# Kernel optimization log

Measured on AMD Instinct MI355X. Metric: run time of the kernel, lower is better.

Reference implementation:

```python
import jax, jax.numpy as jnp
import numpy as np

HID = 128
N_LAYERS = 4
IN_DIM = 2


def _gru_layer(x_seq, W_ih, W_hh, b_ih, b_hh):
    """PyTorch-equivalent single GRU layer.
    x_seq: (T, N, F); W_ih: (3H, F); W_hh: (3H, H); b_ih, b_hh: (3H,)
    Gate order (PyTorch): r, z, n.
    """
    T, N, _ = x_seq.shape
    # precompute input projections for all timesteps: (T, N, 3H)
    gi = jnp.einsum('tnf,gf->tng', x_seq, W_ih) + b_ih

    def step(h, gi_t):
        gh = h @ W_hh.T + b_hh                      # (N, 3H)
        gi_r, gi_z, gi_n = jnp.split(gi_t, 3, axis=-1)
        gh_r, gh_z, gh_n = jnp.split(gh, 3, axis=-1)
        r = jax.nn.sigmoid(gi_r + gh_r)
        z = jax.nn.sigmoid(gi_z + gh_z)
        n = jnp.tanh(gi_n + r * gh_n)
        h_new = (1.0 - z) * n + z * h
        return h_new, h_new

    h0 = jnp.zeros((N, HID), dtype=x_seq.dtype)
    _, out = jax.lax.scan(step, h0, gi)
    return out                                       # (T, N, H)


def setup_inputs() -> dict:
    key = jax.random.key(0)
    ks = jax.random.split(key, 12)
    s = 1.0 / np.sqrt(HID)  # PyTorch GRU init scale
    x = jax.random.normal(ks[0], (512, IN_DIM, 1024), dtype=jnp.float32)
    W_ih0 = jax.random.uniform(ks[1], (3 * HID, IN_DIM), minval=-s, maxval=s)
    W_ih_rest = jax.random.uniform(ks[2], (N_LAYERS - 1, 3 * HID, HID), minval=-s, maxval=s)
    W_hh = jax.random.uniform(ks[3], (N_LAYERS, 3 * HID, HID), minval=-s, maxval=s)
    b_ih = jax.random.uniform(ks[4], (N_LAYERS, 3 * HID), minval=-s, maxval=s)
    b_hh = jax.random.uniform(ks[5], (N_LAYERS, 3 * HID), minval=-s, maxval=s)
    fc1_w = jax.random.uniform(ks[6], (HID, HID), minval=-s, maxval=s)
    fc1_b = jax.random.uniform(ks[7], (HID,), minval=-s, maxval=s)
    fc2_w = jax.random.uniform(ks[8], (3, HID), minval=-s, maxval=s)
    fc2_b = jax.random.uniform(ks[9], (3,), minval=-s, maxval=s)
    return {"x": x, "W_ih0": W_ih0, "W_ih_rest": W_ih_rest, "W_hh": W_hh,
            "b_ih": b_ih, "b_hh": b_hh, "fc1_w": fc1_w, "fc1_b": fc1_b,
            "fc2_w": fc2_w, "fc2_b": fc2_b}


def reference(x, W_ih0, W_ih_rest, W_hh, b_ih, b_hh, fc1_w, fc1_b, fc2_w, fc2_b):
    # x: (B, 2, S) -> transpose(1,2) -> (B, S, 2); GRU (batch_first=False)
    # treats axis0 as time T=B, axis1 as batch N=S.
    h = jnp.transpose(x, (0, 2, 1))                  # (T, N, 2)
    h = _gru_layer(h, W_ih0, W_hh[0], b_ih[0], b_hh[0])
    for l in range(1, N_LAYERS):
        h = _gru_layer(h, W_ih_rest[l - 1], W_hh[l], b_ih[l], b_hh[l])
    # out[:, -1, :] -> last lane along the GRU batch axis: (T, H)
    last = h[:, -1, :]
    hidden = jax.nn.relu(last @ fc1_w.T + fc1_b)
    return hidden @ fc2_w.T + fc2_b                  # (B, 3)
```

## Files before the change

kernel.cpp:

```cpp
#include <hip/hip_runtime.h>
#include <math.h>

#define T_SEQ  512
#define HID    128
#define G3     384
#define NL     4
#define CHUNK  8
#define NCHUNK (T_SEQ / CHUNK)

#define GI_TOT   (NL * T_SEQ * G3)
#define SEQ_TOT  (NL * T_SEQ * HID)
#define FLAG_OFF (GI_TOT + SEQ_TOT)

__device__ __forceinline__ float fsig(float x) {
    float e = __expf(-x);
    return 1.0f / (1.0f + e);
}
__device__ __forceinline__ float ftanh(float x) {
    float ax = fabsf(x);
    float e = __expf(-2.0f * ax);
    float t = (1.0f - e) / (1.0f + e);
    return copysignf(t, x);
}
__device__ __forceinline__ float rdlane(float v, int k) {
    return __uint_as_float(__builtin_amdgcn_readlane(__float_as_uint(v), k));
}


__global__ void init_flags(int* fl) {
    int i = threadIdx.x;
    if (i < 8) fl[i * 16] = (i == 0) ? NCHUNK : 0;
}

__global__ void gi0_kernel(const float* __restrict__ x, const float* __restrict__ Wih0,
                           const float* __restrict__ bih, float* __restrict__ gi) {
    int t = blockIdx.x;
    int g = threadIdx.x;
    float x0 = x[t * 2048 + 1023];
    float x1 = x[t * 2048 + 1024 + 1023];
    gi[t * G3 + g] = bih[g] + Wih0[g * 2 + 0] * x0 + Wih0[g * 2 + 1] * x1;
}

__global__ __launch_bounds__(256, 1) void pipe_kernel(float* __restrict__ ws,
                                                      const float* __restrict__ WihR,
                                                      const float* __restrict__ bih,
                                                      const float* __restrict__ Whh,
                                                      const float* __restrict__ bhh) {
    __shared__ float smem[12288];

    int bid  = blockIdx.x;
    int tid  = threadIdx.x;
    int lane = tid & 63;
    int q    = tid >> 6;
    int row0 = lane * 6;
    int* fl = (int*)(ws + FLAG_OFF);
    bool is_rec = (bid & 1) == 0;
    int  l      = is_rec ? (bid >> 1) : ((bid + 1) >> 1);

    if (is_rec) {
        const float* W   = Whh + (size_t)l * G3 * HID;
        const float* gi  = ws + (size_t)l * T_SEQ * G3;
        float* seq_o     = ws + GI_TOT + (size_t)l * T_SEQ * HID;
        float* aux       = smem + 3072;
        int* in_flag     = &fl[l * 16];
        int* out_flag    = &fl[(4 + l) * 16];

        float w[6][32];
        const float* wbase = W + q * 32;
#pragma unroll
        for (int i = 0; i < 6; i++) {
            const float4* wr = reinterpret_cast<const float4*>(wbase + (size_t)(row0 + i) * HID);
#pragma unroll
            for (int c = 0; c < 8; c++) {
                float4 v = wr[c];
                w[i][c * 4 + 0] = v.x; w[i][c * 4 + 1] = v.y;
                w[i][c * 4 + 2] = v.z; w[i][c * 4 + 3] = v.w;
            }
        }

        int  m  = lane & 31;
        bool p2 = (lane < 32);
        int  j  = q * 32 + m;
        const float* bb = bhh + (size_t)l * G3;
        float br = 0.f, bz = 0.f, bn = 0.f;
        if (p2) { br = bb[j]; bz = bb[HID + j]; bn = bb[2 * HID + j]; }

        float hs[32];
#pragma unroll
        for (int k = 0; k < 32; k++) hs[k] = 0.f;
        float hprev = 0.f;
        float g_r[CHUNK], g_z[CHUNK], g_n[CHUNK];
        int   fseen = 0;

        if (tid == 0) {
            while (__hip_atomic_fetch_add(in_flag, 0, __ATOMIC_RELAXED, __HIP_MEMORY_SCOPE_AGENT) < 1)
                __builtin_amdgcn_s_sleep(2);
        }
        __syncthreads();
        if (p2) {
            const float* gp = gi + j;
#pragma unroll
            for (int s = 0; s < CHUNK; s++) {
                g_r[s] = gp[s * G3];
                g_z[s] = gp[s * G3 + HID];
                g_n[s] = gp[s * G3 + 2 * HID];
            }
        }

        for (int c = 0; c < NCHUNK; c++) {
            int t0 = c * CHUNK;
            bool more = (c + 1 < NCHUNK);
#pragma unroll
            for (int s = 0; s < CHUNK; s++) {
                int t = t0 + s;
                float* psb = smem + (t & 1) * 1536;
                float acc[6];
#pragma unroll
                for (int i = 0; i < 6; i++) {
                    float a0 = 0.f, a1 = 0.f, a2 = 0.f, a3 = 0.f;
#pragma unroll
                    for (int k = 0; k < 32; k += 4) {
                        a0 += w[i][k]     * hs[k];
                        a1 += w[i][k + 1] * hs[k + 1];
                        a2 += w[i][k + 2] * hs[k + 2];
                        a3 += w[i][k + 3] * hs[k + 3];
                    }
                    acc[i] = (a0 + a1) + (a2 + a3);
                }
#pragma unroll
                for (int i = 0; i < 6; i += 2) {
                    float2 p; p.x = acc[i]; p.y = acc[i + 1];
                    *reinterpret_cast<float2*>(&psb[q * G3 + row0 + i]) = p;
                }
                __syncthreads();
                float hn_bc = 0.f;
                if (p2) {
                    float ghr = (psb[j]         + psb[G3 + j])         + (psb[2*G3 + j]         + psb[3*G3 + j]);
                    float ghz = (psb[HID + j]   + psb[G3 + HID + j])   + (psb[2*G3 + HID + j]   + psb[3*G3 + HID + j]);
                    float ghn = (psb[2*HID + j] + psb[G3 + 2*HID + j]) + (psb[2*G3 + 2*HID + j] + psb[3*G3 + 2*HID + j]);
                    float r = fsig(g_r[s] + ghr + br);
                    float z = fsig(g_z[s] + ghz + bz);
                    float n = ftanh(g_n[s] + r * (ghn + bn));
                    float hn = (1.0f - z) * n + z * hprev;
                    hprev = hn;
                    aux[s * HID + j] = hn;
                    hn_bc = hn;
                }
#pragma unroll
                for (int k = 0; k < 32; k++) hs[k] = rdlane(hn_bc, k);
            }
            __syncthreads();
            if (more && tid == 0)
                fseen = __hip_atomic_fetch_add(in_flag, 0, __ATOMIC_RELAXED, __HIP_MEMORY_SCOPE_AGENT);
            {
                float4 v = *reinterpret_cast<const float4*>(&aux[tid * 4]);
                *reinterpret_cast<float4*>(&seq_o[(size_t)t0 * HID + tid * 4]) = v;
            }
            __syncthreads();
            if (tid == 0)
                __hip_atomic_store(out_flag, c + 1, __ATOMIC_RELEASE, __HIP_MEMORY_SCOPE_AGENT);
            if (more && tid == 0) {
                while (fseen < c + 2) {
                    __builtin_amdgcn_s_sleep(2);
                    fseen = __hip_atomic_fetch_add(in_flag, 0, __ATOMIC_RELAXED, __HIP_MEMORY_SCOPE_AGENT);
                }
            }
            __syncthreads();
            if (more && p2) {
                const float* gp = gi + (size_t)(t0 + CHUNK) * G3 + j;
#pragma unroll
                for (int s = 0; s < CHUNK; s++) {
                    g_r[s] = gp[s * G3];
                    g_z[s] = gp[s * G3 + HID];
                    g_n[s] = gp[s * G3 + 2 * HID];
                }
            }
        }
    } else {
        const float* W   = WihR + (size_t)(l - 1) * G3 * HID;
        const float* seq_in = ws + GI_TOT + (size_t)(l - 1) * T_SEQ * HID;
        float* gi_o      = ws + (size_t)l * T_SEQ * G3;
        int* in_flag     = &fl[(4 + (l - 1)) * 16];
        int* out_flag    = &fl[l * 16];

        float w[6][32];
        const float* wbase = W + q * 32;
#pragma unroll
        for (int i = 0; i < 6; i++) {
            const float4* wr = reinterpret_cast<const float4*>(wbase + (size_t)(row0 + i) * HID);
#pragma unroll
            for (int c = 0; c < 8; c++) {
                float4 v = wr[c];
                w[i][c * 4 + 0] = v.x; w[i][c * 4 + 1] = v.y;
                w[i][c * 4 + 2] = v.z; w[i][c * 4 + 3] = v.w;
            }
        }
        int m  = lane & 31;
        int m2 = tid & 31;
        int s2 = tid >> 5;
        const float* bb = bih + (size_t)l * G3;
        float br4[4], bz4[4], bn4[4];
#pragma unroll
        for (int u = 0; u < 4; u++) {
            int jj = u * 32 + m2;
            br4[u] = bb[jj]; bz4[u] = bb[HID + jj]; bn4[u] = bb[2 * HID + jj];
        }

        for (int c = 0; c < NCHUNK; c++) {
            if (tid == 0) {
                while (__hip_atomic_fetch_add(in_flag, 0, __ATOMIC_RELAXED, __HIP_MEMORY_SCOPE_AGENT) < c + 1)
                    __builtin_amdgcn_s_sleep(2);
            }
            __syncthreads();
            int t0 = c * CHUNK;
            float vseq[CHUNK];
            {
                const float* sp = seq_in + (size_t)t0 * HID + q * 32 + m;
#pragma unroll
                for (int s = 0; s < CHUNK; s++) vseq[s] = sp[s * HID];
            }
#pragma unroll
            for (int s = 0; s < CHUNK; s++) {
                float xs[32];
#pragma unroll
                for (int k = 0; k < 32; k++) xs[k] = rdlane(vseq[s], k);
                float acc[6];
#pragma unroll
                for (int i = 0; i < 6; i++) {
                    float a0 = 0.f, a1 = 0.f, a2 = 0.f, a3 = 0.f;
#pragma unroll
                    for (int k = 0; k < 32; k += 4) {
                        a0 += w[i][k]     * xs[k];
                        a1 += w[i][k + 1] * xs[k + 1];
                        a2 += w[i][k + 2] * xs[k + 2];
                        a3 += w[i][k + 3] * xs[k + 3];
                    }
                    acc[i] = (a0 + a1) + (a2 + a3);
                }
                float* pp = smem + s * 1536;
#pragma unroll
                for (int i = 0; i < 6; i += 2) {
                    float2 p; p.x = acc[i]; p.y = acc[i + 1];
                    *reinterpret_cast<float2*>(&pp[q * G3 + row0 + i]) = p;
                }
            }
            __syncthreads();
#pragma unroll
            for (int u = 0; u < 4; u++) {
                int jj = u * 32 + m2;
                const float* pp = smem + s2 * 1536;
                float vr = (pp[jj]         + pp[G3 + jj])         + (pp[2*G3 + jj]         + pp[3*G3 + jj]);
                float vz = (pp[HID + jj]   + pp[G3 + HID + jj])   + (pp[2*G3 + HID + jj]   + pp[3*G3 + HID + jj]);
                float vn = (pp[2*HID + jj] + pp[G3 + 2*HID + jj]) + (pp[2*G3 + 2*HID + jj] + pp[3*G3 + 2*HID + jj]);
                float* gp = gi_o + (size_t)(t0 + s2) * G3;
                gp[jj]           = vr + br4[u];
                gp[HID + jj]     = vz + bz4[u];
                gp[2 * HID + jj] = vn + bn4[u];
            }
            __syncthreads();
            if (tid == 0)
                __hip_atomic_store(out_flag, c + 1, __ATOMIC_RELEASE, __HIP_MEMORY_SCOPE_AGENT);
        }
    }
}

__global__ void fc_kernel(const float* __restrict__ seq, const float* __restrict__ fc1w,
                          const float* __restrict__ fc1b, const float* __restrict__ fc2w,
                          const float* __restrict__ fc2b, float* __restrict__ out) {
    __shared__ float h3[HID];
    __shared__ float hid[HID];
    int t = blockIdx.x;
    int i = threadIdx.x;
    h3[i] = seq[t * HID + i];
    __syncthreads();
    const float4* w4 = reinterpret_cast<const float4*>(fc1w + i * HID);
    const float4* h4 = reinterpret_cast<const float4*>(h3);
    float a0 = 0.f, a1 = 0.f, a2 = 0.f, a3 = 0.f;
#pragma unroll
    for (int k = 0; k < 32; k += 4) {
        float4 w0 = w4[k], w1 = w4[k + 1], w2 = w4[k + 2], w3 = w4[k + 3];
        float4 h0 = h4[k], h1 = h4[k + 1], h2 = h4[k + 2], h3v = h4[k + 3];
        a0 += w0.x * h0.x + w0.y * h0.y + w0.z * h0.z + w0.w * h0.w;
        a1 += w1.x * h1.x + w1.y * h1.y + w1.z * h1.z + w1.w * h1.w;
        a2 += w2.x * h2.x + w2.y * h2.y + w2.z * h2.z + w2.w * h2.w;
        a3 += w3.x * h3v.x + w3.y * h3v.y + w3.z * h3v.z + w3.w * h3v.w;
    }
    float v = fc1b[i] + ((a0 + a1) + (a2 + a3));
    hid[i] = v > 0.0f ? v : 0.0f;
    __syncthreads();
    if (i < 3) {
        const float* w = fc2w + i * HID;
        float s = 0.f;
#pragma unroll
        for (int k = 0; k < HID; k++) s += w[k] * hid[k];
        out[t * 3 + i] = fc2b[i] + s;
    }
}

extern "C" void kernel_launch(void* const* d_in, const int* in_sizes, int n_in,
                              void* d_out, int out_size, void* d_ws, size_t ws_size,
                              hipStream_t stream) {
    const float* x     = (const float*)d_in[0];
    const float* Wih0  = (const float*)d_in[1];
    const float* WihR  = (const float*)d_in[2];
    const float* Whh   = (const float*)d_in[3];
    const float* bih   = (const float*)d_in[4];
    const float* bhh   = (const float*)d_in[5];
    const float* fc1w  = (const float*)d_in[6];
    const float* fc1b  = (const float*)d_in[7];
    const float* fc2w  = (const float*)d_in[8];
    const float* fc2b  = (const float*)d_in[9];
    float* out = (float*)d_out;
    float* ws  = (float*)d_ws;

    int*   flags = (int*)(ws + FLAG_OFF);
    float* gi0   = ws;
    float* seq3  = ws + GI_TOT + (size_t)3 * T_SEQ * HID;

    init_flags<<<1, 64, 0, stream>>>(flags);
    gi0_kernel<<<T_SEQ, G3, 0, stream>>>(x, Wih0, bih, gi0);
    pipe_kernel<<<7, 256, 0, stream>>>(ws, WihR, bih, Whh, bhh);
    fc_kernel<<<T_SEQ, HID, 0, stream>>>(seq3, fc1w, fc1b, fc2w, fc2b, out);
}
```

Baseline: 390.0 us.

## Double pipeline block width to 512 threads, halving per-thread matvec rows

Each block in the layer-pipelined GRU kernel now runs 8 wavefronts instead of 4. The 384 gate rows are split into two halves of 192, so each thread holds 3 weight rows instead of 6, and the GEMV store, aux write and gi_o reduction mappings are adjusted to match. The goal is to shorten the serial per-timestep matvec latency on the recurrence critical path by spreading the work across more waves. In exchange, each __syncthreads now covers twice as many waves, and the gate-update step runs redundantly in both halves.

```diff
diff --git a/kernel.cpp b/kernel.cpp
--- a/kernel.cpp
+++ b/kernel.cpp
@@ -41,7 +41,7 @@
     gi[t * G3 + g] = bih[g] + Wih0[g * 2 + 0] * x0 + Wih0[g * 2 + 1] * x1;
 }
 
-__global__ __launch_bounds__(256, 1) void pipe_kernel(float* __restrict__ ws,
+__global__ __launch_bounds__(512, 1) void pipe_kernel(float* __restrict__ ws,
                                                       const float* __restrict__ WihR,
                                                       const float* __restrict__ bih,
                                                       const float* __restrict__ Whh,
@@ -51,8 +51,10 @@
     int bid  = blockIdx.x;
     int tid  = threadIdx.x;
     int lane = tid & 63;
-    int q    = tid >> 6;
-    int row0 = lane * 6;
+    int wv   = tid >> 6;
+    int q    = wv & 3;
+    int half = wv >> 2;
+    int row0 = half * 192 + lane * 3;
     int* fl = (int*)(ws + FLAG_OFF);
     bool is_rec = (bid & 1) == 0;
     int  l      = is_rec ? (bid >> 1) : ((bid + 1) >> 1);
@@ -65,10 +67,10 @@
         int* in_flag     = &fl[l * 16];
         int* out_flag    = &fl[(4 + l) * 16];
 
-        float w[6][32];
+        float w[3][32];
         const float* wbase = W + q * 32;
 #pragma unroll
-        for (int i = 0; i < 6; i++) {
+        for (int i = 0; i < 3; i++) {
             const float4* wr = reinterpret_cast<const float4*>(wbase + (size_t)(row0 + i) * HID);
 #pragma unroll
             for (int c = 0; c < 8; c++) {
@@ -114,9 +116,9 @@
             for (int s = 0; s < CHUNK; s++) {
                 int t = t0 + s;
                 float* psb = smem + (t & 1) * 1536;
-                float acc[6];
-#pragma unroll
-                for (int i = 0; i < 6; i++) {
+                float acc[3];
+#pragma unroll
+                for (int i = 0; i < 3; i++) {
                     float a0 = 0.f, a1 = 0.f, a2 = 0.f, a3 = 0.f;
 #pragma unroll
                     for (int k = 0; k < 32; k += 4) {
@@ -128,10 +130,7 @@
                     acc[i] = (a0 + a1) + (a2 + a3);
                 }
 #pragma unroll
-                for (int i = 0; i < 6; i += 2) {
-                    float2 p; p.x = acc[i]; p.y = acc[i + 1];
-                    *reinterpret_cast<float2*>(&psb[q * G3 + row0 + i]) = p;
-                }
+                for (int i = 0; i < 3; i++) psb[q * G3 + row0 + i] = acc[i];
                 __syncthreads();
                 float hn_bc = 0.f;
                 if (p2) {
@@ -143,7 +142,7 @@
                     float n = ftanh(g_n[s] + r * (ghn + bn));
                     float hn = (1.0f - z) * n + z * hprev;
                     hprev = hn;
-                    aux[s * HID + j] = hn;
+                    if (half == 0) aux[s * HID + j] = hn;
                     hn_bc = hn;
                 }
 #pragma unroll
@@ -153,8 +152,8 @@
             if (more && tid == 0)
                 fseen = __hip_atomic_fetch_add(in_flag, 0, __ATOMIC_RELAXED, __HIP_MEMORY_SCOPE_AGENT);
             {
-                float4 v = *reinterpret_cast<const float4*>(&aux[tid * 4]);
-                *reinterpret_cast<float4*>(&seq_o[(size_t)t0 * HID + tid * 4]) = v;
+                float2 v = *reinterpret_cast<const float2*>(&aux[tid * 2]);
+                *reinterpret_cast<float2*>(&seq_o[(size_t)t0 * HID + tid * 2]) = v;
             }
             __syncthreads();
             if (tid == 0)
@@ -183,10 +182,10 @@
         int* in_flag     = &fl[(4 + (l - 1)) * 16];
         int* out_flag    = &fl[l * 16];
 
-        float w[6][32];
+        float w[3][32];
         const float* wbase = W + q * 32;
 #pragma unroll
-        for (int i = 0; i < 6; i++) {
+        for (int i = 0; i < 3; i++) {
             const float4* wr = reinterpret_cast<const float4*>(wbase + (size_t)(row0 + i) * HID);
 #pragma unroll
             for (int c = 0; c < 8; c++) {
@@ -196,14 +195,14 @@
             }
         }
         int m  = lane & 31;
-        int m2 = tid & 31;
-        int s2 = tid >> 5;
+        int m3 = tid & 63;
+        int s2 = tid >> 6;
         const float* bb = bih + (size_t)l * G3;
-        float br4[4], bz4[4], bn4[4];
-#pragma unroll
-        for (int u = 0; u < 4; u++) {
-            int jj = u * 32 + m2;
-            br4[u] = bb[jj]; bz4[u] = bb[HID + jj]; bn4[u] = bb[2 * HID + jj];
+        float br2[2], bz2[2], bn2[2];
+#pragma unroll
+        for (int u = 0; u < 2; u++) {
+            int jj = u * 64 + m3;
+            br2[u] = bb[jj]; bz2[u] = bb[HID + jj]; bn2[u] = bb[2 * HID + jj];
         }
 
         for (int c = 0; c < NCHUNK; c++) {
@@ -224,9 +223,9 @@
                 float xs[32];
 #pragma unroll
                 for (int k = 0; k < 32; k++) xs[k] = rdlane(vseq[s], k);
-                float acc[6];
-#pragma unroll
-                for (int i = 0; i < 6; i++) {
+                float acc[3];
+#pragma unroll
+                for (int i = 0; i < 3; i++) {
                     float a0 = 0.f, a1 = 0.f, a2 = 0.f, a3 = 0.f;
 #pragma unroll
                     for (int k = 0; k < 32; k += 4) {
@@ -239,23 +238,20 @@
                 }
                 float* pp = smem + s * 1536;
 #pragma unroll
-                for (int i = 0; i < 6; i += 2) {
-                    float2 p; p.x = acc[i]; p.y = acc[i + 1];
-                    *reinterpret_cast<float2*>(&pp[q * G3 + row0 + i]) = p;
-                }
-            }
-            __syncthreads();
-#pragma unroll
-            for (int u = 0; u < 4; u++) {
-                int jj = u * 32 + m2;
+                for (int i = 0; i < 3; i++) pp[q * G3 + row0 + i] = acc[i];
+            }
+            __syncthreads();
+#pragma unroll
+            for (int u = 0; u < 2; u++) {
+                int jj = u * 64 + m3;
                 const float* pp = smem + s2 * 1536;
                 float vr = (pp[jj]         + pp[G3 + jj])         + (pp[2*G3 + jj]         + pp[3*G3 + jj]);
                 float vz = (pp[HID + jj]   + pp[G3 + HID + jj])   + (pp[2*G3 + HID + jj]   + pp[3*G3 + HID + jj]);
                 float vn = (pp[2*HID + jj] + pp[G3 + 2*HID + jj]) + (pp[2*G3 + 2*HID + jj] + pp[3*G3 + 2*HID + jj]);
                 float* gp = gi_o + (size_t)(t0 + s2) * G3;
-                gp[jj]           = vr + br4[u];
-                gp[HID + jj]     = vz + bz4[u];
-                gp[2 * HID + jj] = vn + bn4[u];
+                gp[jj]           = vr + br2[u];
+                gp[HID + jj]     = vz + bz2[u];
+                gp[2 * HID + jj] = vn + bn2[u];
             }
             __syncthreads();
             if (tid == 0)
@@ -319,6 +315,6 @@
 
     init_flags<<<1, 64, 0, stream>>>(flags);
     gi0_kernel<<<T_SEQ, G3, 0, stream>>>(x, Wih0, bih, gi0);
-    pipe_kernel<<<7, 256, 0, stream>>>(ws, WihR, bih, Whh, bhh);
+    pipe_kernel<<<7, 512, 0, stream>>>(ws, WihR, bih, Whh, bhh);
     fc_kernel<<<T_SEQ, HID, 0, stream>>>(seq3, fc1w, fc1b, fc2w, fc2b, out);
 }
```

After: 524.9 us. 34.6% more time.
